# Performance work log

Hardware: AMD Instinct MI355X
Metric: run time of the kernel (lower is better)

Reference implementation:

```python
import jax, jax.numpy as jnp
import numpy as np


def setup_inputs() -> dict:
    key = jax.random.key(0)
    k1, k2, k3, k4 = jax.random.split(key, 4)
    B, C, T, H, W = 2, 64, 8, 48, 48
    C2 = C // 2
    x_in = jax.random.normal(k1, (B, C, T, H, W), dtype=jnp.float32)
    # per-time-slice 1x1 conv weights (theta/phi pairs), kaiming-ish scale
    theta_w = jax.random.normal(k2, (T, C2, C), dtype=jnp.float32) / np.sqrt(C)
    phi_w = jax.random.normal(k3, (T, C2, C), dtype=jnp.float32) / np.sqrt(C)
    out_w = jax.random.normal(k4, (C, C), dtype=jnp.float32) / np.sqrt(C)
    return {"x_in": x_in, "theta_w": theta_w, "phi_w": phi_w, "out_w": out_w}


def reference(x_in, theta_w, phi_w, out_w):
    B, C, T, H, W = x_in.shape
    C2 = theta_w.shape[1]
    P = H * W
    # [B, T, C, P] layout: flatten spatial, move time next to batch
    x = jnp.transpose(x_in, (0, 2, 1, 3, 4)).reshape(B, T, C, P)
    # per-slice 1x1 convs == per-slice channel matmuls with slice-specific weights
    theta = jnp.einsum("toc,btcp->btop", theta_w, x)  # [B,T,C2,P]
    phi = jnp.einsum("toc,btcp->btop", phi_w, x)      # [B,T,C2,P]
    scale = 1.0 / jnp.sqrt(jnp.asarray(C2, dtype=x_in.dtype))
    scores = jnp.einsum("btcp,btcq->btpq", theta, phi) * scale  # [B,T,P,P]
    attn = jax.nn.softmax(scores, axis=-1)
    f = jnp.einsum("btpq,btcq->btcp", attn, x)  # value = raw x, [B,T,C,P]
    # conv_out: 1x1x1 Conv3d (pointwise over channels), then residual
    out = jnp.einsum("oc,btcp->btop", out_w, f)
    out = jnp.transpose(out.reshape(B, T, C, H, W), (0, 2, 1, 3, 4))
    return out + x_in
```

## Files before the change

### kernel.cpp

```cpp
#include <hip/hip_runtime.h>
#include <hip/hip_bf16.h>

#define CC 64
#define TT 8
#define PP 2304
#define C2 32
#define BT 16
#define NKT 36
#define HKT 18
#define SCALE2 0.25503486f

using h8 = __attribute__((ext_vector_type(8))) _Float16;
using h4 = __attribute__((ext_vector_type(4))) _Float16;
using f4 = __attribute__((ext_vector_type(4))) float;

#if __has_builtin(__builtin_amdgcn_exp2f)
#define EXP2(v) __builtin_amdgcn_exp2f(v)
#else
#define EXP2(v) exp2f(v)
#endif

#define SWIZ_BT(xcd, g) ((xcd) + 8 * ((g) & 1))
#define SWIZ_PT(g) ((g) >> 1)


__global__ __launch_bounds__(256) void k_prep(
    const float* __restrict__ x, const float* __restrict__ tw,
    const float* __restrict__ pw, _Float16* __restrict__ thf,
    _Float16* __restrict__ rec) {
  const int qt = SWIZ_PT(blockIdx.y), bt = SWIZ_BT(blockIdx.x, blockIdx.y);
  const int b = bt >> 3, t = bt & 7;
  const int tid = threadIdx.x;
  const int wv = tid >> 6, lane = tid & 63;
  const int quad = lane >> 4, l15 = lane & 15;

  __shared__ __align__(16) float x_s[64][68];
  __shared__ __align__(16) _Float16 th_s[4][16][32];
  __shared__ __align__(16) _Float16 ph_s[4][16][32];

  const size_t xslice = ((size_t)b * CC * TT + t) * PP;
  const int qg0 = qt * 64;

  {
    const int qq = tid & 63;
    const int c0 = (tid >> 6) * 16;
#pragma unroll
    for (int i = 0; i < 16; i++) {
      int c = c0 + i;
      x_s[qq][c] = x[xslice + (size_t)c * (TT * PP) + qg0 + qq];
    }
  }
  __syncthreads();

  h8 bx[2];
#pragma unroll
  for (int ks = 0; ks < 2; ks++) {
    const float* row = &x_s[wv * 16 + l15][ks * 32 + quad * 8];
    float4 u0 = *reinterpret_cast<const float4*>(row);
    float4 u1 = *reinterpret_cast<const float4*>(row + 4);
    bx[ks][0] = (_Float16)u0.x; bx[ks][1] = (_Float16)u0.y;
    bx[ks][2] = (_Float16)u0.z; bx[ks][3] = (_Float16)u0.w;
    bx[ks][4] = (_Float16)u1.x; bx[ks][5] = (_Float16)u1.y;
    bx[ks][6] = (_Float16)u1.z; bx[ks][7] = (_Float16)u1.w;
  }

  const float* twt = tw + t * C2 * CC;
  const float* pwt = pw + t * C2 * CC;
  const f4 zero = {0.f, 0.f, 0.f, 0.f};
  f4 accT[2] = {zero, zero}, accP[2] = {zero, zero};
#pragma unroll
  for (int mt = 0; mt < 2; mt++)
#pragma unroll
    for (int ks = 0; ks < 2; ks++) {
      const float* wr = twt + (mt * 16 + l15) * CC + ks * 32 + quad * 8;
      const float* pr = pwt + (mt * 16 + l15) * CC + ks * 32 + quad * 8;
      float4 a0 = *reinterpret_cast<const float4*>(wr);
      float4 a1 = *reinterpret_cast<const float4*>(wr + 4);
      float4 p0 = *reinterpret_cast<const float4*>(pr);
      float4 p1 = *reinterpret_cast<const float4*>(pr + 4);
      h8 at = {(_Float16)a0.x, (_Float16)a0.y, (_Float16)a0.z, (_Float16)a0.w,
               (_Float16)a1.x, (_Float16)a1.y, (_Float16)a1.z, (_Float16)a1.w};
      h8 ap = {(_Float16)p0.x, (_Float16)p0.y, (_Float16)p0.z, (_Float16)p0.w,
               (_Float16)p1.x, (_Float16)p1.y, (_Float16)p1.z, (_Float16)p1.w};
      accT[mt] =
          __builtin_amdgcn_mfma_f32_16x16x32_f16(at, bx[ks], accT[mt], 0, 0, 0);
      accP[mt] =
          __builtin_amdgcn_mfma_f32_16x16x32_f16(ap, bx[ks], accP[mt], 0, 0, 0);
    }

#pragma unroll
  for (int mt = 0; mt < 2; mt++) {
    h4 tv, pv;
#pragma unroll
    for (int r = 0; r < 4; r++) {
      tv[r] = (_Float16)(accT[mt][r] * SCALE2);
      pv[r] = (_Float16)accP[mt][r];
    }
    *reinterpret_cast<h4*>(&th_s[wv][l15][mt * 16 + quad * 4]) = tv;
    *reinterpret_cast<h4*>(&ph_s[wv][l15][mt * 16 + quad * 4]) = pv;
  }

  h8 tfrag = *reinterpret_cast<const h8*>(&th_s[wv][l15][quad * 8]);
  *reinterpret_cast<h8*>(
      thf + (((size_t)(bt * NKT + qt) * 4 + wv) * 64 + lane) * 8) = tfrag;

  _Float16* rb = rec + (size_t)(bt * NKT + qt) * 6144;
  h8 pfrag = *reinterpret_cast<const h8*>(&ph_s[wv][l15][quad * 8]);
  *reinterpret_cast<h8*>(rb + wv * 512 + lane * 8) = pfrag;

#pragma unroll
  for (int ctp = 0; ctp < 2; ctp++) {
    h8 v;
#pragma unroll
    for (int j = 0; j < 4; j++) {
      v[j] = (_Float16)x_s[wv * 16 + quad * 4 + j][(2 * ctp) * 16 + l15];
      v[4 + j] = (_Float16)x_s[wv * 16 + quad * 4 + j][(2 * ctp + 1) * 16 + l15];
    }
    *reinterpret_cast<h8*>(rb + 2048 + (wv * 2 + ctp) * 512 + lane * 8) = v;
  }
}

__global__ __launch_bounds__(512, 4) void k_attn(
    const float* __restrict__ x, const _Float16* __restrict__ thf,
    const _Float16* __restrict__ rec, const float* __restrict__ ow,
    float* __restrict__ out) {
  const int pt = SWIZ_PT(blockIdx.y), bt = SWIZ_BT(blockIdx.x, blockIdx.y);
  const int b = bt >> 3, t = bt & 7;
  const int tid = threadIdx.x;
  const int wv = tid >> 6, lane = tid & 63;
  const int quad = lane >> 4, l15 = lane & 15;
  const int qg = wv & 3, kg = wv >> 2;

  __shared__ __align__(16) char smem[49152];
  _Float16* stage = reinterpret_cast<_Float16*>(smem);
  float* exch = reinterpret_cast<float*>(smem);
  float* out_s = reinterpret_cast<float*>(smem + 20480);

  const h8 b_th = *reinterpret_cast<const h8*>(
      thf + (((size_t)(bt * NKT + pt) * 4 + qg) * 64 + lane) * 8);

  const _Float16* recb = rec + (size_t)bt * NKT * 6144;

  const int m0 = wv * 3;
  int ch_tile[3], ch_off[3];
#pragma unroll
  for (int j = 0; j < 3; j++) {
    int m = m0 + j;
    ch_tile[j] = m / 12;
    ch_off[j] = (m % 12) * 512 + lane * 8;
  }

  int4 v[3];
#pragma unroll
  for (int j = 0; j < 3; j++) {
    v[j] = *reinterpret_cast<const int4*>(recb +
                                          (size_t)(ch_tile[j] * HKT) * 6144 +
                                          ch_off[j]);
    *reinterpret_cast<int4*>(stage + ch_tile[j] * 6144 + ch_off[j]) = v[j];
  }

  const f4 zero = {0.f, 0.f, 0.f, 0.f};
  f4 O[4] = {zero, zero, zero, zero};
  float l_sum = 0.f;

  for (int i = 0; i < HKT; i++) {
    __syncthreads();
    const _Float16* cur = stage + (i & 1) * 12288 + kg * 6144;

    if (i < HKT - 1) {
#pragma unroll
      for (int j = 0; j < 3; j++)
        v[j] = *reinterpret_cast<const int4*>(
            recb + (size_t)(ch_tile[j] * HKT + i + 1) * 6144 + ch_off[j]);
    }

    h8 aphi[4];
#pragma unroll
    for (int nt = 0; nt < 4; nt++)
      aphi[nt] = *reinterpret_cast<const h8*>(cur + nt * 512 + lane * 8);
    f4 s[4];
#pragma unroll
    for (int nt = 0; nt < 4; nt++)
      s[nt] =
          __builtin_amdgcn_mfma_f32_16x16x32_f16(aphi[nt], b_th, zero, 0, 0, 0);

#pragma unroll
    for (int nt = 0; nt < 4; nt++) {
      h4 bw;
#pragma unroll
      for (int r = 0; r < 4; r++) {
        float w = EXP2(s[nt][r]);
        l_sum += w;
        bw[r] = (_Float16)w;
      }
#pragma unroll
      for (int ctp = 0; ctp < 2; ctp++) {
        h8 xx = *reinterpret_cast<const h8*>(cur + 2048 +
                                             (nt * 2 + ctp) * 512 + lane * 8);
        h4 a0 = __builtin_shufflevector(xx, xx, 0, 1, 2, 3);
        h4 a1 = __builtin_shufflevector(xx, xx, 4, 5, 6, 7);
        O[2 * ctp] =
            __builtin_amdgcn_mfma_f32_16x16x16f16(a0, bw, O[2 * ctp], 0, 0, 0);
        O[2 * ctp + 1] = __builtin_amdgcn_mfma_f32_16x16x16f16(
            a1, bw, O[2 * ctp + 1], 0, 0, 0);
      }
    }

    if (i < HKT - 1) {
#pragma unroll
      for (int j = 0; j < 3; j++)
        *reinterpret_cast<int4*>(stage + ((i + 1) & 1) * 12288 +
                                 ch_tile[j] * 6144 + ch_off[j]) = v[j];
    }
  }

  l_sum += __shfl_xor(l_sum, 16);
  l_sum += __shfl_xor(l_sum, 32);

  __syncthreads();

  if (kg == 1) {
#pragma unroll
    for (int k = 0; k < 16; k++)
      exch[(qg * 17 + k) * 64 + lane] = O[k >> 2][k & 3];
    exch[(qg * 17 + 16) * 64 + lane] = l_sum;
  }
  __syncthreads();

  if (kg == 0) {
#pragma unroll
    for (int k = 0; k < 16; k++)
      O[k >> 2][k & 3] += exch[(qg * 17 + k) * 64 + lane];
    const float inv = 1.f / (l_sum + exch[(qg * 17 + 16) * 64 + lane]);

    h4 bf[4];
#pragma unroll
    for (int ct = 0; ct < 4; ct++)
#pragma unroll
      for (int r = 0; r < 4; r++) bf[ct][r] = (_Float16)(O[ct][r] * inv);

    f4 D3[4] = {zero, zero, zero, zero};
#pragma unroll
    for (int mt = 0; mt < 4; mt++)
#pragma unroll
      for (int ct = 0; ct < 4; ct++) {
        const float* wrow =
            ow + (size_t)(mt * 16 + l15) * CC + ct * 16 + quad * 4;
        float4 u = *reinterpret_cast<const float4*>(wrow);
        h4 aw = {(_Float16)u.x, (_Float16)u.y, (_Float16)u.z, (_Float16)u.w};
        D3[mt] =
            __builtin_amdgcn_mfma_f32_16x16x16f16(aw, bf[ct], D3[mt], 0, 0, 0);
      }

#pragma unroll
    for (int mt = 0; mt < 4; mt++)
#pragma unroll
      for (int r = 0; r < 4; r++)
        out_s[(mt * 16 + quad * 4 + r) * 68 + qg * 16 + l15] = D3[mt][r];
  }
  __syncthreads();

  const int co = tid >> 3;
  const int psub = (tid & 7) * 8;
  const size_t gbase = ((size_t)(b * CC + co) * TT + t) * PP + pt * 64 + psub;
#pragma unroll
  for (int jj = 0; jj < 2; jj++) {
    float4 vo =
        *reinterpret_cast<const float4*>(&out_s[co * 68 + psub + jj * 4]);
    float4 xr = *reinterpret_cast<const float4*>(&x[gbase + jj * 4]);
    vo.x += xr.x; vo.y += xr.y; vo.z += xr.z; vo.w += xr.w;
    *reinterpret_cast<float4*>(&out[gbase + jj * 4]) = vo;
  }
}

extern "C" void kernel_launch(void* const* d_in, const int* in_sizes, int n_in,
                              void* d_out, int out_size, void* d_ws,
                              size_t ws_size, hipStream_t stream) {
  (void)in_sizes; (void)n_in; (void)out_size; (void)ws_size;
  const float* x = (const float*)d_in[0];
  const float* tw = (const float*)d_in[1];
  const float* pw = (const float*)d_in[2];
  const float* ow = (const float*)d_in[3];
  float* out = (float*)d_out;

  _Float16* thf = (_Float16*)d_ws;
  _Float16* rec = thf + (size_t)BT * NKT * 4 * 64 * 8;

  k_prep<<<dim3(8, 72), 256, 0, stream>>>(x, tw, pw, thf, rec);
  k_attn<<<dim3(8, 72), 512, 0, stream>>>(x, thf, rec, ow, out);
}
```

Baseline: 109.8 us.

## Halve attention block to 4 waves, each handling two query subtiles

The attention kernel now runs with 256 threads (4 waves) instead of 512. Each wave processes two 16-query subtiles, so every loaded phi and x fragment from shared memory feeds twice as many MFMAs. The intent is fewer LDS reads per MFMA and fewer waves contending at each barrier. In exchange each wave uses more registers (doubled accumulators and staging loads), and there are fewer waves per block to hide latency.

```diff
diff --git a/kernel.cpp b/kernel.cpp
--- a/kernel.cpp
+++ b/kernel.cpp
@@ -120,7 +120,7 @@
   }
 }
 
-__global__ __launch_bounds__(512, 4) void k_attn(
+__global__ __launch_bounds__(256, 3) void k_attn(
     const float* __restrict__ x, const _Float16* __restrict__ thf,
     const _Float16* __restrict__ rec, const float* __restrict__ ow,
     float* __restrict__ out) {
@@ -129,39 +129,40 @@
   const int tid = threadIdx.x;
   const int wv = tid >> 6, lane = tid & 63;
   const int quad = lane >> 4, l15 = lane & 15;
-  const int qg = wv & 3, kg = wv >> 2;
+  const int qg = wv & 1, kg = wv >> 1;
 
   __shared__ __align__(16) char smem[49152];
   _Float16* stage = reinterpret_cast<_Float16*>(smem);
   float* exch = reinterpret_cast<float*>(smem);
   float* out_s = reinterpret_cast<float*>(smem + 20480);
 
-  const h8 b_th = *reinterpret_cast<const h8*>(
-      thf + (((size_t)(bt * NKT + pt) * 4 + qg) * 64 + lane) * 8);
+  h8 b_th[2];
+#pragma unroll
+  for (int ps = 0; ps < 2; ps++)
+    b_th[ps] = *reinterpret_cast<const h8*>(
+        thf + (((size_t)(bt * NKT + pt) * 4 + qg * 2 + ps) * 64 + lane) * 8);
 
   const _Float16* recb = rec + (size_t)bt * NKT * 6144;
 
-  const int m0 = wv * 3;
-  int ch_tile[3], ch_off[3];
-#pragma unroll
-  for (int j = 0; j < 3; j++) {
-    int m = m0 + j;
+  int ch_tile[6], ch_off[6];
+#pragma unroll
+  for (int j = 0; j < 6; j++) {
+    int m = wv * 6 + j;
     ch_tile[j] = m / 12;
     ch_off[j] = (m % 12) * 512 + lane * 8;
   }
 
-  int4 v[3];
-#pragma unroll
-  for (int j = 0; j < 3; j++) {
-    v[j] = *reinterpret_cast<const int4*>(recb +
-                                          (size_t)(ch_tile[j] * HKT) * 6144 +
-                                          ch_off[j]);
+  int4 v[6];
+#pragma unroll
+  for (int j = 0; j < 6; j++) {
+    v[j] = *reinterpret_cast<const int4*>(
+        recb + (size_t)(ch_tile[j] * HKT) * 6144 + ch_off[j]);
     *reinterpret_cast<int4*>(stage + ch_tile[j] * 6144 + ch_off[j]) = v[j];
   }
 
   const f4 zero = {0.f, 0.f, 0.f, 0.f};
-  f4 O[4] = {zero, zero, zero, zero};
-  float l_sum = 0.f;
+  f4 O[2][4] = {{zero, zero, zero, zero}, {zero, zero, zero, zero}};
+  float l_sum[2] = {0.f, 0.f};
 
   for (int i = 0; i < HKT; i++) {
     __syncthreads();
@@ -169,7 +170,7 @@
 
     if (i < HKT - 1) {
 #pragma unroll
-      for (int j = 0; j < 3; j++)
+      for (int j = 0; j < 6; j++)
         v[j] = *reinterpret_cast<const int4*>(
             recb + (size_t)(ch_tile[j] * HKT + i + 1) * 6144 + ch_off[j]);
     }
@@ -178,93 +179,111 @@
 #pragma unroll
     for (int nt = 0; nt < 4; nt++)
       aphi[nt] = *reinterpret_cast<const h8*>(cur + nt * 512 + lane * 8);
-    f4 s[4];
+    f4 s[4][2];
 #pragma unroll
     for (int nt = 0; nt < 4; nt++)
-      s[nt] =
-          __builtin_amdgcn_mfma_f32_16x16x32_f16(aphi[nt], b_th, zero, 0, 0, 0);
+#pragma unroll
+      for (int ps = 0; ps < 2; ps++)
+        s[nt][ps] = __builtin_amdgcn_mfma_f32_16x16x32_f16(aphi[nt], b_th[ps],
+                                                           zero, 0, 0, 0);
 
 #pragma unroll
     for (int nt = 0; nt < 4; nt++) {
-      h4 bw;
-#pragma unroll
-      for (int r = 0; r < 4; r++) {
-        float w = EXP2(s[nt][r]);
-        l_sum += w;
-        bw[r] = (_Float16)w;
-      }
+      h4 bw[2];
+#pragma unroll
+      for (int ps = 0; ps < 2; ps++)
+#pragma unroll
+        for (int r = 0; r < 4; r++) {
+          float w = EXP2(s[nt][ps][r]);
+          l_sum[ps] += w;
+          bw[ps][r] = (_Float16)w;
+        }
 #pragma unroll
       for (int ctp = 0; ctp < 2; ctp++) {
-        h8 xx = *reinterpret_cast<const h8*>(cur + 2048 +
-                                             (nt * 2 + ctp) * 512 + lane * 8);
+        h8 xx = *reinterpret_cast<const h8*>(cur + 2048 + (nt * 2 + ctp) * 512 +
+                                             lane * 8);
         h4 a0 = __builtin_shufflevector(xx, xx, 0, 1, 2, 3);
         h4 a1 = __builtin_shufflevector(xx, xx, 4, 5, 6, 7);
-        O[2 * ctp] =
-            __builtin_amdgcn_mfma_f32_16x16x16f16(a0, bw, O[2 * ctp], 0, 0, 0);
-        O[2 * ctp + 1] = __builtin_amdgcn_mfma_f32_16x16x16f16(
-            a1, bw, O[2 * ctp + 1], 0, 0, 0);
+#pragma unroll
+        for (int ps = 0; ps < 2; ps++) {
+          O[ps][2 * ctp] = __builtin_amdgcn_mfma_f32_16x16x16f16(
+              a0, bw[ps], O[ps][2 * ctp], 0, 0, 0);
+          O[ps][2 * ctp + 1] = __builtin_amdgcn_mfma_f32_16x16x16f16(
+              a1, bw[ps], O[ps][2 * ctp + 1], 0, 0, 0);
+        }
       }
     }
 
     if (i < HKT - 1) {
 #pragma unroll
-      for (int j = 0; j < 3; j++)
+      for (int j = 0; j < 6; j++)
         *reinterpret_cast<int4*>(stage + ((i + 1) & 1) * 12288 +
                                  ch_tile[j] * 6144 + ch_off[j]) = v[j];
     }
   }
 
-  l_sum += __shfl_xor(l_sum, 16);
-  l_sum += __shfl_xor(l_sum, 32);
+#pragma unroll
+  for (int ps = 0; ps < 2; ps++) {
+    l_sum[ps] += __shfl_xor(l_sum[ps], 16);
+    l_sum[ps] += __shfl_xor(l_sum[ps], 32);
+  }
 
   __syncthreads();
 
   if (kg == 1) {
 #pragma unroll
-    for (int k = 0; k < 16; k++)
-      exch[(qg * 17 + k) * 64 + lane] = O[k >> 2][k & 3];
-    exch[(qg * 17 + 16) * 64 + lane] = l_sum;
+    for (int ps = 0; ps < 2; ps++) {
+#pragma unroll
+      for (int k = 0; k < 16; k++)
+        exch[((qg * 2 + ps) * 17 + k) * 64 + lane] = O[ps][k >> 2][k & 3];
+      exch[((qg * 2 + ps) * 17 + 16) * 64 + lane] = l_sum[ps];
+    }
   }
   __syncthreads();
 
   if (kg == 0) {
 #pragma unroll
-    for (int k = 0; k < 16; k++)
-      O[k >> 2][k & 3] += exch[(qg * 17 + k) * 64 + lane];
-    const float inv = 1.f / (l_sum + exch[(qg * 17 + 16) * 64 + lane]);
-
-    h4 bf[4];
-#pragma unroll
-    for (int ct = 0; ct < 4; ct++)
-#pragma unroll
-      for (int r = 0; r < 4; r++) bf[ct][r] = (_Float16)(O[ct][r] * inv);
-
-    f4 D3[4] = {zero, zero, zero, zero};
-#pragma unroll
-    for (int mt = 0; mt < 4; mt++)
-#pragma unroll
-      for (int ct = 0; ct < 4; ct++) {
-        const float* wrow =
-            ow + (size_t)(mt * 16 + l15) * CC + ct * 16 + quad * 4;
-        float4 u = *reinterpret_cast<const float4*>(wrow);
-        h4 aw = {(_Float16)u.x, (_Float16)u.y, (_Float16)u.z, (_Float16)u.w};
-        D3[mt] =
-            __builtin_amdgcn_mfma_f32_16x16x16f16(aw, bf[ct], D3[mt], 0, 0, 0);
-      }
-
-#pragma unroll
-    for (int mt = 0; mt < 4; mt++)
-#pragma unroll
-      for (int r = 0; r < 4; r++)
-        out_s[(mt * 16 + quad * 4 + r) * 68 + qg * 16 + l15] = D3[mt][r];
+    for (int ps = 0; ps < 2; ps++) {
+#pragma unroll
+      for (int k = 0; k < 16; k++)
+        O[ps][k >> 2][k & 3] += exch[((qg * 2 + ps) * 17 + k) * 64 + lane];
+      const float inv =
+          1.f / (l_sum[ps] + exch[((qg * 2 + ps) * 17 + 16) * 64 + lane]);
+
+      h4 bf[4];
+#pragma unroll
+      for (int ct = 0; ct < 4; ct++)
+#pragma unroll
+        for (int r = 0; r < 4; r++) bf[ct][r] = (_Float16)(O[ps][ct][r] * inv);
+
+      f4 D3[4] = {zero, zero, zero, zero};
+#pragma unroll
+      for (int mt = 0; mt < 4; mt++)
+#pragma unroll
+        for (int ct = 0; ct < 4; ct++) {
+          const float* wrow =
+              ow + (size_t)(mt * 16 + l15) * CC + ct * 16 + quad * 4;
+          float4 u = *reinterpret_cast<const float4*>(wrow);
+          h4 aw = {(_Float16)u.x, (_Float16)u.y, (_Float16)u.z, (_Float16)u.w};
+          D3[mt] =
+              __builtin_amdgcn_mfma_f32_16x16x16f16(aw, bf[ct], D3[mt], 0, 0, 0);
+        }
+
+#pragma unroll
+      for (int mt = 0; mt < 4; mt++)
+#pragma unroll
+        for (int r = 0; r < 4; r++)
+          out_s[(mt * 16 + quad * 4 + r) * 68 + (qg * 2 + ps) * 16 + l15] =
+              D3[mt][r];
+    }
   }
   __syncthreads();
 
-  const int co = tid >> 3;
-  const int psub = (tid & 7) * 8;
+  const int co = tid >> 2;
+  const int psub = (tid & 3) * 16;
   const size_t gbase = ((size_t)(b * CC + co) * TT + t) * PP + pt * 64 + psub;
 #pragma unroll
-  for (int jj = 0; jj < 2; jj++) {
+  for (int jj = 0; jj < 4; jj++) {
     float4 vo =
         *reinterpret_cast<const float4*>(&out_s[co * 68 + psub + jj * 4]);
     float4 xr = *reinterpret_cast<const float4*>(&x[gbase + jj * 4]);
@@ -287,5 +306,5 @@
   _Float16* rec = thf + (size_t)BT * NKT * 4 * 64 * 8;
 
   k_prep<<<dim3(8, 72), 256, 0, stream>>>(x, tw, pw, thf, rec);
-  k_attn<<<dim3(8, 72), 512, 0, stream>>>(x, thf, rec, ow, out);
+  k_attn<<<dim3(8, 72), 256, 0, stream>>>(x, thf, rec, ow, out);
 }
```

Measured after the change: 113.5 us. +3.4%, slower.
